# Performance work log

Hardware: AMD Instinct MI355X
Metric: run time of the kernel (lower is better)

Reference implementation:

```python
import jax, jax.numpy as jnp
import numpy as np

N = 100000      # total nodes (flattened batch)
E = 640000      # total edges
D = 128         # in_channels
SIM_THR = 0.2   # pt_dict['sim_pt']
DEG_THR = 3.0   # pt_dict['degree_pt']
PT_THRESHOLD = 0.1  # edge-pruning cosine threshold
EPS = 1e-8      # F.cosine_similarity eps


def _glorot(key, shape):
    a = np.sqrt(6.0 / (shape[-2] + shape[-1]))
    return jax.random.uniform(key, shape, jnp.float32, -a, a)


def setup_inputs() -> dict:
    key = jax.random.key(0)
    k1, k2, k3, k4, k5 = jax.random.split(key, 5)
    x = jax.random.normal(k1, (N, D), jnp.float32)
    edge_index = jax.random.randint(k2, (2, E), 0, N, dtype=jnp.int32)
    p_sim = _glorot(k3, (1, D))
    p_deg = _glorot(k4, (1, D))
    p_other = _glorot(k5, (1, D))
    return {"x": x, "edge_index": edge_index, "p_sim": p_sim, "p_deg": p_deg, "p_other": p_other}


def reference(x, edge_index, p_sim, p_deg, p_other):
    n = x.shape[0]
    row, col = edge_index[0], edge_index[1]

    # --- sim_pt: per-edge cosine of raw features, scatter-add to dst, degree-normalize ---
    x_norm = x / jnp.sqrt(jnp.sum(x * x, axis=1, keepdims=True))          # [N, D]
    e = jnp.sum(x_norm[row] * x_norm[col], axis=1)                         # [E]
    c = jax.ops.segment_sum(e, col, num_segments=n)                        # [N]
    deg = jax.ops.segment_sum(jnp.ones_like(e), col, num_segments=n)       # [N]
    # torch: c/deg -> nan for deg==0, nan <= thr is False; +inf gives the same mask, safely.
    csim = jnp.where(deg > 0, c / jnp.maximum(deg, 1.0), jnp.inf)
    mask_sim = csim <= SIM_THR                                             # [N]

    # --- degree_pt ---
    mask_deg = deg <= DEG_THR                                              # [N]

    # --- other_pt == 'all': nodes that got no prompt so far ---
    mask_other = ~(mask_sim | mask_deg)                                    # [N]

    # g_mutiftpt_record: [N, 3, D], slot filled with its prompt row where mask else 0
    masks = jnp.stack([mask_sim, mask_deg, mask_other], axis=1)            # [N, 3]
    prompts = jnp.concatenate([p_sim, p_deg, p_other], axis=0)             # [3, D]
    record = masks[:, :, None].astype(x.dtype) * prompts[None, :, :]       # [N, 3, D]

    # use_attention=False branch: mean over non-padding (all-nonzero) slots
    wo_pad = jnp.all(record != 0, axis=-1)                                 # [N, 3]
    plen = jnp.sum(wo_pad, axis=1, keepdims=True).astype(x.dtype)          # [N, 1]
    final = jnp.where(plen > 0, record.sum(axis=1) / jnp.maximum(plen, 1.0), 0.0)  # [N, D]

    x_new = x + final                                                      # add_pt

    # edge pruning by cosine similarity of prompted features (F.cosine_similarity, eps=1e-8)
    nrm = jnp.sqrt(jnp.sum(x_new * x_new, axis=1))                         # [N]
    na = jnp.maximum(nrm[row], EPS)
    nb = jnp.maximum(nrm[col], EPS)
    cos = jnp.sum(x_new[row] * x_new[col], axis=1) / (na * nb)             # [E]
    keep_edges = cos >= PT_THRESHOLD                                       # [E] bool mask (edge list is static-shape; mask instead of compaction)
    return x_new, keep_edges
```

## Files before the change

kernel.cpp:

```cpp
#include <hip/hip_runtime.h>
#include <hip/hip_bf16.h>
#include <hip/hip_fp8.h>
#include <math.h>

#define D_DIM 128
#define SIM_THR 0.2f
#define DEG_THR 3.0f
#define PT_THR 0.1
#define EPS_CS 1e-8
#define NODE_MARGIN 0.022f
#define PRUNE_MARGIN 0.022f
#define PK 4294967296.0

typedef unsigned short u16;
typedef unsigned int u32;

#define WS_NEED 8092900

__device__ __forceinline__ float bf2f(u16 u) {
    return __uint_as_float(((u32)u) << 16);
}
__device__ __forceinline__ float f8f(u32 v) {
    __hip_fp8_e4m3 t;
    t.__x = (__hip_fp8_storage_t)v;
    return (float)t;
}
__device__ __forceinline__ u16 f2bf(float f) {
    __hip_bfloat16 b = __float2bfloat16(f);
    return *(u16*)&b;
}

__global__ void node_pre_fp8(const float* __restrict__ x,
                             const float* __restrict__ ps,
                             const float* __restrict__ pd,
                             const float* __restrict__ po,
                             u32* __restrict__ x8d,
                             float* __restrict__ nx,
                             float* __restrict__ rs,
                             float* __restrict__ rd,
                             float* __restrict__ ro,
                             double* __restrict__ cd,
                             u32* __restrict__ bitmap, int nbmw,
                             int* __restrict__ flags,
                             float* __restrict__ G, int N) {
    int g = threadIdx.x >> 5;
    int lane = threadIdx.x & 31;
    int n = blockIdx.x * 8 + g;
    int gid = blockIdx.x * 256 + threadIdx.x;
    if (gid < nbmw) bitmap[gid] = 0u;
    if (n < N) {
        int off = lane * 4;
        const float4 v = *(const float4*)(x + (size_t)n * D_DIM + off);
        const float4 s = *(const float4*)(ps + off);
        const float4 d = *(const float4*)(pd + off);
        const float4 o = *(const float4*)(po + off);
        float sq = v.x * v.x + v.y * v.y + v.z * v.z + v.w * v.w;
        float drs = v.x * s.x + v.y * s.y + v.z * s.z + v.w * s.w;
        float drd = v.x * d.x + v.y * d.y + v.z * d.z + v.w * d.w;
        float dro = v.x * o.x + v.y * o.y + v.z * o.z + v.w * o.w;
        for (int m = 16; m; m >>= 1) {
            sq += __shfl_xor(sq, m, 32);
            drs += __shfl_xor(drs, m, 32);
            drd += __shfl_xor(drd, m, 32);
            dro += __shfl_xor(dro, m, 32);
        }
        float nrm = sqrtf(sq);
        float inv = 1.0f / nrm;
        __hip_fp8_e4m3 q0(v.x * inv), q1(v.y * inv), q2(v.z * inv), q3(v.w * inv);
        u32 packed = (u32)q0.__x | ((u32)q1.__x << 8) |
                     ((u32)q2.__x << 16) | ((u32)q3.__x << 24);
        x8d[(size_t)n * 32 + lane] = packed;
        if (lane == 0) {
            nx[n] = nrm;
            rs[n] = drs;
            rd[n] = drd;
            ro[n] = dro;
            cd[n] = 0.0;
        }
    }
    if (blockIdx.x == 0 && threadIdx.x < 64) {
        int t = threadIdx.x;
        float s0 = ps[t], s1 = ps[t + 64];
        float d0 = pd[t], d1 = pd[t + 64];
        float o0 = po[t], o1 = po[t + 64];
        float ss = s0 * s0 + s1 * s1;
        float sd = s0 * d0 + s1 * d1;
        float so = s0 * o0 + s1 * o1;
        float dd = d0 * d0 + d1 * d1;
        float dO = d0 * o0 + d1 * o1;
        float oo = o0 * o0 + o1 * o1;
        for (int m = 32; m; m >>= 1) {
            ss += __shfl_xor(ss, m);
            sd += __shfl_xor(sd, m);
            so += __shfl_xor(so, m);
            dd += __shfl_xor(dd, m);
            dO += __shfl_xor(dO, m);
            oo += __shfl_xor(oo, m);
        }
        unsigned long long zs = __ballot(s0 == 0.0f || s1 == 0.0f);
        unsigned long long zd = __ballot(d0 == 0.0f || d1 == 0.0f);
        unsigned long long zo = __ballot(o0 == 0.0f || o1 == 0.0f);
        if (t == 0) {
            flags[0] = (zs == 0ull);
            flags[1] = (zd == 0ull);
            flags[2] = (zo == 0ull);
            G[0] = ss; G[1] = sd; G[2] = so;
            G[3] = sd; G[4] = dd; G[5] = dO;
            G[6] = so; G[7] = dO; G[8] = oo;
        }
    }
}

__global__ void edge_sim_fp8(const u32* __restrict__ x8d,
                             const int* __restrict__ ei,
                             double* __restrict__ cd,
                             u16* __restrict__ e_arr,
                             int E) {
    int lane = threadIdx.x & 31;
    int grp = blockIdx.x * 8 + (threadIdx.x >> 5);
    int base = grp * 4;
    if (base >= E) return;

    int r[4], c4[4];
    #pragma unroll
    for (int k = 0; k < 4; ++k) {
        int e = base + k;
        int src = (e < E) ? e : base;
        r[k] = ei[src];
        c4[k] = ei[E + src];
    }
    u32 a[4], b[4];
    #pragma unroll
    for (int k = 0; k < 4; ++k) {
        a[k] = x8d[(size_t)r[k] * 32 + lane];
        b[k] = x8d[(size_t)c4[k] * 32 + lane];
    }
    float d[4];
    #pragma unroll
    for (int k = 0; k < 4; ++k) {
        d[k] = f8f(a[k] & 255u) * f8f(b[k] & 255u) +
               f8f((a[k] >> 8) & 255u) * f8f((b[k] >> 8) & 255u) +
               f8f((a[k] >> 16) & 255u) * f8f((b[k] >> 16) & 255u) +
               f8f(a[k] >> 24) * f8f(b[k] >> 24);
    }
    for (int m = 16; m; m >>= 1) {
        #pragma unroll
        for (int k = 0; k < 4; ++k) d[k] += __shfl_xor(d[k], m, 32);
    }
    if (lane < 4) {
        int e = base + lane;
        if (e < E) {
            float dv = (lane == 0) ? d[0] : (lane == 1) ? d[1]
                     : (lane == 2) ? d[2] : d[3];
            e_arr[e] = f2bf(dv);
            atomicAdd(&cd[c4[lane]], (double)dv + PK);
        }
    }
}

__global__ void node_prompt_kernel(const float* __restrict__ x,
                                   const double* __restrict__ cd,
                                   const float* __restrict__ ps,
                                   const float* __restrict__ pd,
                                   const float* __restrict__ po,
                                   const int* __restrict__ flags,
                                   const float* __restrict__ nx,
                                   const float* __restrict__ rs,
                                   const float* __restrict__ rd,
                                   const float* __restrict__ ro,
                                   float* __restrict__ xn,
                                   double* __restrict__ na,
                                   float* __restrict__ pack,
                                   u32* __restrict__ bitmap,
                                   float* __restrict__ cfix, int N) {
    int g = threadIdx.x >> 5;
    int lane = threadIdx.x & 31;
    int n = blockIdx.x * 8 + g;
    if (n >= N) return;
    double v = cd[n];
    double degd = floor(v * (1.0 / PK) + 0.5);
    float dg = (float)degd;
    float cc = (float)(v - degd * PK);
    float csim = (dg > 0.0f) ? (cc / fmaxf(dg, 1.0f)) : INFINITY;
    bool ms = (csim <= SIM_THR);
    bool md = (dg <= DEG_THR);
    bool mo = !(ms || md);
    int plen = (ms && flags[0]) + (md && flags[1]) + (mo && flags[2]);
    float invp = (plen > 0) ? (1.0f / (float)plen) : 0.0f;

    int off = lane * 4;
    const float4 xv = *(const float4*)(x + (size_t)n * D_DIM + off);
    const float4 s  = *(const float4*)(ps + off);
    const float4 dd = *(const float4*)(pd + off);
    const float4 o  = *(const float4*)(po + off);

    float4 f;
    f.x = (ms ? s.x : 0.0f) + (md ? dd.x : 0.0f) + (mo ? o.x : 0.0f);
    f.y = (ms ? s.y : 0.0f) + (md ? dd.y : 0.0f) + (mo ? o.y : 0.0f);
    f.z = (ms ? s.z : 0.0f) + (md ? dd.z : 0.0f) + (mo ? o.z : 0.0f);
    f.w = (ms ? s.w : 0.0f) + (md ? dd.w : 0.0f) + (mo ? o.w : 0.0f);

    float4 r;
    r.x = xv.x + f.x * invp;
    r.y = xv.y + f.y * invp;
    r.z = xv.z + f.z * invp;
    r.w = xv.w + f.w * invp;

    *(float4*)(xn + (size_t)n * D_DIM + off) = r;

    double sq = (double)r.x * r.x + (double)r.y * r.y + (double)r.z * r.z + (double)r.w * r.w;
    for (int m = 16; m; m >>= 1) sq += __shfl_xor(sq, m, 32);
    if (lane == 0) {
        double nrm = sqrt(sq);
        double nad = (nrm > EPS_CS) ? nrm : EPS_CS;
        na[n] = nad;
        float as = ms ? invp : 0.0f;
        float ad = md ? invp : 0.0f;
        float ao = mo ? invp : 0.0f;
        *(float4*)(pack + (size_t)n * 8)     = make_float4(rs[n], rd[n], ro[n], nx[n]);
        *(float4*)(pack + (size_t)n * 8 + 4) = make_float4(as, ad, ao, (float)(1.0 / nad));
        if (dg > 0.0f && fabsf(csim - SIM_THR) < NODE_MARGIN) {
            cfix[n] = 0.0f;
            atomicOr(&bitmap[n >> 5], 1u << (n & 31));
        }
    }
}

__global__ void edge_fix_scan(const float* __restrict__ x,
                              const int* __restrict__ ei,
                              const float* __restrict__ nx,
                              const u32* __restrict__ bitmap,
                              float* __restrict__ cfix, int E) {
    int e = blockIdx.x * 256 + threadIdx.x;
    if (e >= E) return;
    int col = ei[E + e];
    if (!((bitmap[col >> 5] >> (col & 31)) & 1u)) return;
    int row = ei[e];
    const float4* xr = (const float4*)(x + (size_t)row * D_DIM);
    const float4* xc = (const float4*)(x + (size_t)col * D_DIM);
    double s = 0.0;
    for (int i = 0; i < 32; ++i) {
        float4 a = xr[i], b = xc[i];
        s += (double)a.x * b.x + (double)a.y * b.y +
             (double)a.z * b.z + (double)a.w * b.w;
    }
    float ev = (float)(s / ((double)nx[row] * (double)nx[col]));
    atomicAdd(&cfix[col], ev);
}

__global__ void node_fix_kernel(const float* __restrict__ x,
                                const double* __restrict__ cd,
                                const float* __restrict__ cfix,
                                const u32* __restrict__ bitmap,
                                const float* __restrict__ ps,
                                const float* __restrict__ pd,
                                const float* __restrict__ po,
                                const int* __restrict__ flags,
                                const float* __restrict__ nx,
                                const float* __restrict__ rs,
                                const float* __restrict__ rd,
                                const float* __restrict__ ro,
                                float* __restrict__ xn,
                                double* __restrict__ na,
                                float* __restrict__ pack, int N) {
    int g = threadIdx.x >> 5;
    int lane = threadIdx.x & 31;
    int n = blockIdx.x * 8 + g;
    if (n >= N) return;
    if (!((bitmap[n >> 5] >> (n & 31)) & 1u)) return;

    double v = cd[n];
    double degd = floor(v * (1.0 / PK) + 0.5);
    float dg = (float)degd;
    float csim = cfix[n] / fmaxf(dg, 1.0f);
    bool ms = (csim <= SIM_THR);
    bool md = (dg <= DEG_THR);
    bool mo = !(ms || md);
    int plen = (ms && flags[0]) + (md && flags[1]) + (mo && flags[2]);
    float invp = (plen > 0) ? (1.0f / (float)plen) : 0.0f;

    int off = lane * 4;
    const float4 xv = *(const float4*)(x + (size_t)n * D_DIM + off);
    const float4 s  = *(const float4*)(ps + off);
    const float4 dd = *(const float4*)(pd + off);
    const float4 o  = *(const float4*)(po + off);

    float4 f;
    f.x = (ms ? s.x : 0.0f) + (md ? dd.x : 0.0f) + (mo ? o.x : 0.0f);
    f.y = (ms ? s.y : 0.0f) + (md ? dd.y : 0.0f) + (mo ? o.y : 0.0f);
    f.z = (ms ? s.z : 0.0f) + (md ? dd.z : 0.0f) + (mo ? o.z : 0.0f);
    f.w = (ms ? s.w : 0.0f) + (md ? dd.w : 0.0f) + (mo ? o.w : 0.0f);

    float4 r;
    r.x = xv.x + f.x * invp;
    r.y = xv.y + f.y * invp;
    r.z = xv.z + f.z * invp;
    r.w = xv.w + f.w * invp;

    *(float4*)(xn + (size_t)n * D_DIM + off) = r;

    double sq = (double)r.x * r.x + (double)r.y * r.y + (double)r.z * r.z + (double)r.w * r.w;
    for (int m = 16; m; m >>= 1) sq += __shfl_xor(sq, m, 32);
    if (lane == 0) {
        double nrm = sqrt(sq);
        double nad = (nrm > EPS_CS) ? nrm : EPS_CS;
        na[n] = nad;
        float as = ms ? invp : 0.0f;
        float ad = md ? invp : 0.0f;
        float ao = mo ? invp : 0.0f;
        *(float4*)(pack + (size_t)n * 8)     = make_float4(rs[n], rd[n], ro[n], nx[n]);
        *(float4*)(pack + (size_t)n * 8 + 4) = make_float4(as, ad, ao, (float)(1.0 / nad));
    }
}

__global__ void edge_prune_fused(const int* __restrict__ ei,
                                 const u16* __restrict__ e_arr,
                                 const float* __restrict__ pack,
                                 const float* __restrict__ G,
                                 const float* __restrict__ xn,
                                 const double* __restrict__ na,
                                 float* __restrict__ keep, int E) {
    __shared__ int s_list[256];
    __shared__ int s_cnt;
    int tid = threadIdx.x;
    if (tid == 0) s_cnt = 0;
    __syncthreads();

    int e = blockIdx.x * 256 + tid;
    if (e < E) {
        int i = ei[e], j = ei[E + e];
        const float4 ri = *(const float4*)(pack + (size_t)i * 8);
        const float4 ai = *(const float4*)(pack + (size_t)i * 8 + 4);
        const float4 rj = *(const float4*)(pack + (size_t)j * 8);
        const float4 aj = *(const float4*)(pack + (size_t)j * 8 + 4);
        float ev = bf2f(e_arr[e]);
        float dot = ev * ri.w * rj.w
                  + aj.x * ri.x + aj.y * ri.y + aj.z * ri.z
                  + ai.x * rj.x + ai.y * rj.y + ai.z * rj.z;
        dot += ai.x * (G[0] * aj.x + G[1] * aj.y + G[2] * aj.z)
             + ai.y * (G[3] * aj.x + G[4] * aj.y + G[5] * aj.z)
             + ai.z * (G[6] * aj.x + G[7] * aj.y + G[8] * aj.z);
        float cosv = dot * ai.w * aj.w;
        keep[e] = (cosv >= 0.1f) ? 1.0f : 0.0f;
        if (fabsf(cosv - 0.1f) < PRUNE_MARGIN) {
            int idx = atomicAdd(&s_cnt, 1);
            if (idx < 256) {
                s_list[idx] = e;
            } else {
                const float4* xr = (const float4*)(xn + (size_t)i * D_DIM);
                const float4* xc = (const float4*)(xn + (size_t)j * D_DIM);
                double sd = 0.0;
                for (int it = 0; it < 32; ++it) {
                    float4 a = xr[it], b = xc[it];
                    sd += (double)a.x * b.x + (double)a.y * b.y +
                          (double)a.z * b.z + (double)a.w * b.w;
                }
                double cs = sd / (na[i] * na[j]);
                keep[e] = (cs >= PT_THR) ? 1.0f : 0.0f;
            }
        }
    }
    __syncthreads();

    int cnt = s_cnt < 256 ? s_cnt : 256;
    int lane = tid & 31;
    int grp = tid >> 5;
    for (int it = grp; it < cnt; it += 8) {
        int ee = s_list[it];
        int row = ei[ee], col = ei[E + ee];
        const float4 a = *(const float4*)(xn + (size_t)row * D_DIM + lane * 4);
        const float4 b = *(const float4*)(xn + (size_t)col * D_DIM + lane * 4);
        double d = (double)a.x * b.x + (double)a.y * b.y +
                   (double)a.z * b.z + (double)a.w * b.w;
        for (int m = 16; m; m >>= 1) d += __shfl_xor(d, m, 32);
        if (lane == 0) {
            double cs = d / (na[row] * na[col]);
            keep[ee] = (cs >= PT_THR) ? 1.0f : 0.0f;
        }
    }
}

__global__ void node_pre_bf16(const float* __restrict__ x,
                              const float* __restrict__ ps,
                              const float* __restrict__ pd,
                              const float* __restrict__ po,
                              u16* __restrict__ xnorm,
                              double* __restrict__ cd,
                              int* __restrict__ flags, int N) {
    int g = threadIdx.x >> 5;
    int lane = threadIdx.x & 31;
    int n = blockIdx.x * 8 + g;
    if (n < N) {
        int off = lane * 4;
        const float4 v = *(const float4*)(x + (size_t)n * D_DIM + off);
        float sq = v.x * v.x + v.y * v.y + v.z * v.z + v.w * v.w;
        for (int m = 16; m; m >>= 1) sq += __shfl_xor(sq, m, 32);
        float inv = 1.0f / sqrtf(sq);
        *(ushort4*)(xnorm + (size_t)n * D_DIM + off) =
            make_ushort4(f2bf(v.x * inv), f2bf(v.y * inv), f2bf(v.z * inv), f2bf(v.w * inv));
        if (lane == 0) cd[n] = 0.0;
    }
    if (blockIdx.x == 0 && threadIdx.x < 64) {
        int t = threadIdx.x;
        unsigned long long zs = __ballot(ps[t] == 0.0f || ps[t + 64] == 0.0f);
        unsigned long long zd = __ballot(pd[t] == 0.0f || pd[t + 64] == 0.0f);
        unsigned long long zo = __ballot(po[t] == 0.0f || po[t + 64] == 0.0f);
        if (t == 0) {
            flags[0] = (zs == 0ull);
            flags[1] = (zd == 0ull);
            flags[2] = (zo == 0ull);
        }
    }
}

__global__ void edge_sim_bf16(const u16* __restrict__ xnorm,
                              const int* __restrict__ ei,
                              double* __restrict__ cd, int E) {
    int lane = threadIdx.x & 31;
    int grp = blockIdx.x * 8 + (threadIdx.x >> 5);
    int base = grp * 4;
    if (base >= E) return;
    int r[4], c4[4];
    #pragma unroll
    for (int k = 0; k < 4; ++k) {
        int e = base + k;
        int src = (e < E) ? e : base;
        r[k] = ei[src];
        c4[k] = ei[E + src];
    }
    float d[4];
    #pragma unroll
    for (int k = 0; k < 4; ++k) {
        ushort4 a = *(const ushort4*)(xnorm + (size_t)r[k] * D_DIM + lane * 4);
        ushort4 b = *(const ushort4*)(xnorm + (size_t)c4[k] * D_DIM + lane * 4);
        d[k] = bf2f(a.x) * bf2f(b.x) + bf2f(a.y) * bf2f(b.y) +
               bf2f(a.z) * bf2f(b.z) + bf2f(a.w) * bf2f(b.w);
    }
    for (int m = 16; m; m >>= 1) {
        #pragma unroll
        for (int k = 0; k < 4; ++k) d[k] += __shfl_xor(d[k], m, 32);
    }
    if (lane < 4) {
        int e = base + lane;
        if (e < E) {
            float dv = (lane == 0) ? d[0] : (lane == 1) ? d[1]
                     : (lane == 2) ? d[2] : d[3];
            atomicAdd(&cd[c4[lane]], (double)dv + PK);
        }
    }
}

__global__ void node_prompt_fb(const float* __restrict__ x,
                               const double* __restrict__ cd,
                               const float* __restrict__ ps,
                               const float* __restrict__ pd,
                               const float* __restrict__ po,
                               const int* __restrict__ flags,
                               float* __restrict__ xn,
                               double* __restrict__ na, int N) {
    int g = threadIdx.x >> 5;
    int lane = threadIdx.x & 31;
    int n = blockIdx.x * 8 + g;
    if (n >= N) return;
    double v = cd[n];
    double degd = floor(v * (1.0 / PK) + 0.5);
    float dg = (float)degd;
    float cc = (float)(v - degd * PK);
    float csim = (dg > 0.0f) ? (cc / fmaxf(dg, 1.0f)) : INFINITY;
    bool ms = (csim <= SIM_THR);
    bool md = (dg <= DEG_THR);
    bool mo = !(ms || md);
    int plen = (ms && flags[0]) + (md && flags[1]) + (mo && flags[2]);
    float invp = (plen > 0) ? (1.0f / (float)plen) : 0.0f;
    int off = lane * 4;
    const float4 xv = *(const float4*)(x + (size_t)n * D_DIM + off);
    const float4 s  = *(const float4*)(ps + off);
    const float4 dd = *(const float4*)(pd + off);
    const float4 o  = *(const float4*)(po + off);
    float4 r;
    r.x = xv.x + ((ms ? s.x : 0.0f) + (md ? dd.x : 0.0f) + (mo ? o.x : 0.0f)) * invp;
    r.y = xv.y + ((ms ? s.y : 0.0f) + (md ? dd.y : 0.0f) + (mo ? o.y : 0.0f)) * invp;
    r.z = xv.z + ((ms ? s.z : 0.0f) + (md ? dd.z : 0.0f) + (mo ? o.z : 0.0f)) * invp;
    r.w = xv.w + ((ms ? s.w : 0.0f) + (md ? dd.w : 0.0f) + (mo ? o.w : 0.0f)) * invp;
    *(float4*)(xn + (size_t)n * D_DIM + off) = r;
    double sq = (double)r.x * r.x + (double)r.y * r.y + (double)r.z * r.z + (double)r.w * r.w;
    for (int m = 16; m; m >>= 1) sq += __shfl_xor(sq, m, 32);
    if (lane == 0) {
        double nrm = sqrt(sq);
        na[n] = (nrm > EPS_CS) ? nrm : EPS_CS;
    }
}

__global__ void edge_prune_exact(const float* __restrict__ xn,
                                 const int* __restrict__ ei,
                                 const double* __restrict__ na,
                                 float* __restrict__ keep, int E) {
    int lane = threadIdx.x & 31;
    int grp = blockIdx.x * 8 + (threadIdx.x >> 5);
    int e0 = grp * 2, e1 = e0 + 1;
    if (e0 >= E) return;
    bool has1 = (e1 < E);
    int row0 = ei[e0], col0 = ei[E + e0];
    int row1 = has1 ? ei[e1] : row0;
    int col1 = has1 ? ei[E + e1] : col0;
    const float4 a0 = *(const float4*)(xn + (size_t)row0 * D_DIM + lane * 4);
    const float4 b0 = *(const float4*)(xn + (size_t)col0 * D_DIM + lane * 4);
    const float4 a1 = *(const float4*)(xn + (size_t)row1 * D_DIM + lane * 4);
    const float4 b1 = *(const float4*)(xn + (size_t)col1 * D_DIM + lane * 4);
    double d0 = (double)a0.x * b0.x + (double)a0.y * b0.y +
                (double)a0.z * b0.z + (double)a0.w * b0.w;
    double d1 = (double)a1.x * b1.x + (double)a1.y * b1.y +
                (double)a1.z * b1.z + (double)a1.w * b1.w;
    for (int m = 16; m; m >>= 1) {
        d0 += __shfl_xor(d0, m, 32);
        d1 += __shfl_xor(d1, m, 32);
    }
    if (lane == 0) {
        keep[e0] = ((d0 / (na[row0] * na[col0])) >= PT_THR) ? 1.0f : 0.0f;
    } else if (lane == 1 && has1) {
        keep[e1] = ((d1 / (na[row1] * na[col1])) >= PT_THR) ? 1.0f : 0.0f;
    }
}

extern "C" void kernel_launch(void* const* d_in, const int* in_sizes, int n_in,
                              void* d_out, int out_size, void* d_ws, size_t ws_size,
                              hipStream_t stream) {
    const float* x  = (const float*)d_in[0];
    const int*   ei = (const int*)d_in[1];
    const float* ps = (const float*)d_in[2];
    const float* pd = (const float*)d_in[3];
    const float* po = (const float*)d_in[4];

    const int N = in_sizes[0] / D_DIM;
    const int E = in_sizes[1] / 2;

    float* xn   = (float*)d_out;
    float* keep = (float*)d_out + (size_t)N * D_DIM;

    char* ws = (char*)d_ws;
    const int nodeBlocks = (N + 7) / 8;
    const int nbmw = (N + 31) / 32;

    if (ws_size >= (size_t)WS_NEED) {
        double* cd    = (double*)(ws + 0);
        double* na    = (double*)(ws + 800000);
        float* nx     = (float*)(ws + 1600000);
        float* rs     = (float*)(ws + 2000000);
        float* rd     = (float*)(ws + 2400000);
        float* ro     = (float*)(ws + 2800000);
        u16*   e_arr  = (u16*)(ws + 3200000);
        float* pack   = (float*)(ws + 4480000);
        float* cfix   = (float*)(ws + 7680000);
        u32*   bitmap = (u32*)(ws + 8080000);
        int*   flags  = (int*)(ws + 8092800);
        float* G      = (float*)(ws + 8092816);
        u32*   x8d    = (u32*)d_out;

        node_pre_fp8<<<nodeBlocks, 256, 0, stream>>>(x, ps, pd, po, x8d, nx, rs, rd, ro,
                                                     cd, bitmap, nbmw, flags, G, N);
        edge_sim_fp8<<<(E + 31) / 32, 256, 0, stream>>>(x8d, ei, cd, e_arr, E);
        node_prompt_kernel<<<nodeBlocks, 256, 0, stream>>>(x, cd, ps, pd, po, flags,
                                                           nx, rs, rd, ro,
                                                           xn, na, pack, bitmap, cfix, N);
        edge_fix_scan<<<(E + 255) / 256, 256, 0, stream>>>(x, ei, nx, bitmap, cfix, E);
        node_fix_kernel<<<nodeBlocks, 256, 0, stream>>>(x, cd, cfix, bitmap, ps, pd, po,
                                                        flags, nx, rs, rd, ro,
                                                        xn, na, pack, N);
        edge_prune_fused<<<(E + 255) / 256, 256, 0, stream>>>(ei, e_arr, pack, G,
                                                              xn, na, keep, E);
    } else {
        double* cd    = (double*)(ws + 0);
        double* na    = (double*)(ws + 800000);
        int*    flags = (int*)(ws + 1600000);
        u16*    xnorm = (u16*)d_out;

        node_pre_bf16<<<nodeBlocks, 256, 0, stream>>>(x, ps, pd, po, xnorm, cd, flags, N);
        edge_sim_bf16<<<(E + 31) / 32, 256, 0, stream>>>(xnorm, ei, cd, E);
        node_prompt_fb<<<nodeBlocks, 256, 0, stream>>>(x, cd, ps, pd, po, flags, xn, na, N);
        edge_prune_exact<<<(E + 15) / 16, 256, 0, stream>>>(xn, ei, na, keep, E);
    }
}
```

Baseline: 115.6 us.

## Switch edge cosine to per-row scaled int8 with sdot4 and skip empty fix passes

Result: faster. 108.6 us (-6.0%).

```diff
diff --git a/kernel.cpp b/kernel.cpp
--- a/kernel.cpp
+++ b/kernel.cpp
@@ -1,6 +1,5 @@
 #include <hip/hip_runtime.h>
 #include <hip/hip_bf16.h>
-#include <hip/hip_fp8.h>
 #include <math.h>
 
 #define D_DIM 128
@@ -8,46 +7,55 @@
 #define DEG_THR 3.0f
 #define PT_THR 0.1
 #define EPS_CS 1e-8
-#define NODE_MARGIN 0.022f
-#define PRUNE_MARGIN 0.022f
+#define NODE_MARGIN 8e-3f
+#define PRUNE_MARGIN 8e-3f
 #define PK 4294967296.0
 
 typedef unsigned short u16;
 typedef unsigned int u32;
 
-#define WS_NEED 8092900
+#define WS_NEED 9772860
 
 __device__ __forceinline__ float bf2f(u16 u) {
     return __uint_as_float(((u32)u) << 16);
-}
-__device__ __forceinline__ float f8f(u32 v) {
-    __hip_fp8_e4m3 t;
-    t.__x = (__hip_fp8_storage_t)v;
-    return (float)t;
 }
 __device__ __forceinline__ u16 f2bf(float f) {
     __hip_bfloat16 b = __float2bfloat16(f);
     return *(u16*)&b;
 }
-
-__global__ void node_pre_fp8(const float* __restrict__ x,
-                             const float* __restrict__ ps,
-                             const float* __restrict__ pd,
-                             const float* __restrict__ po,
-                             u32* __restrict__ x8d,
-                             float* __restrict__ nx,
-                             float* __restrict__ rs,
-                             float* __restrict__ rd,
-                             float* __restrict__ ro,
-                             double* __restrict__ cd,
-                             u32* __restrict__ bitmap, int nbmw,
-                             int* __restrict__ flags,
-                             float* __restrict__ G, int N) {
+__device__ __forceinline__ int dot4i8(u32 a, u32 b, int acc) {
+#if __has_builtin(__builtin_amdgcn_sdot4)
+    return __builtin_amdgcn_sdot4(a, b, acc, false);
+#else
+    acc += (int)(char)(a) * (int)(char)(b);
+    acc += (int)(char)(a >> 8) * (int)(char)(b >> 8);
+    acc += (int)(char)(a >> 16) * (int)(char)(b >> 16);
+    acc += (int)(char)(a >> 24) * (int)(char)(b >> 24);
+    return acc;
+#endif
+}
+
+__global__ void node_pre_i8(const float* __restrict__ x,
+                            const float* __restrict__ ps,
+                            const float* __restrict__ pd,
+                            const float* __restrict__ po,
+                            u32* __restrict__ x8d,
+                            float* __restrict__ nx,
+                            float* __restrict__ rs,
+                            float* __restrict__ rd,
+                            float* __restrict__ ro,
+                            float* __restrict__ sc,
+                            double* __restrict__ cd,
+                            u32* __restrict__ bitmap, int nbmw,
+                            int* __restrict__ flags,
+                            float* __restrict__ G,
+                            int* __restrict__ flagcnt, int N) {
     int g = threadIdx.x >> 5;
     int lane = threadIdx.x & 31;
     int n = blockIdx.x * 8 + g;
     int gid = blockIdx.x * 256 + threadIdx.x;
     if (gid < nbmw) bitmap[gid] = 0u;
+    if (gid == 0) *flagcnt = 0;
     if (n < N) {
         int off = lane * 4;
         const float4 v = *(const float4*)(x + (size_t)n * D_DIM + off);
@@ -66,15 +74,24 @@
         }
         float nrm = sqrtf(sq);
         float inv = 1.0f / nrm;
-        __hip_fp8_e4m3 q0(v.x * inv), q1(v.y * inv), q2(v.z * inv), q3(v.w * inv);
-        u32 packed = (u32)q0.__x | ((u32)q1.__x << 8) |
-                     ((u32)q2.__x << 16) | ((u32)q3.__x << 24);
+        float v0 = v.x * inv, v1 = v.y * inv, v2 = v.z * inv, v3 = v.w * inv;
+        float mx = fmaxf(fmaxf(fabsf(v0), fabsf(v1)), fmaxf(fabsf(v2), fabsf(v3)));
+        for (int m = 16; m; m >>= 1) mx = fmaxf(mx, __shfl_xor(mx, m, 32));
+        float scale = fmaxf(mx, 1e-20f) * (1.0f / 127.0f);
+        float isc = 1.0f / scale;
+        int q0 = __float2int_rn(v0 * isc);
+        int q1 = __float2int_rn(v1 * isc);
+        int q2 = __float2int_rn(v2 * isc);
+        int q3 = __float2int_rn(v3 * isc);
+        u32 packed = ((u32)q0 & 255u) | (((u32)q1 & 255u) << 8) |
+                     (((u32)q2 & 255u) << 16) | (((u32)q3 & 255u) << 24);
         x8d[(size_t)n * 32 + lane] = packed;
         if (lane == 0) {
             nx[n] = nrm;
             rs[n] = drs;
             rd[n] = drd;
             ro[n] = dro;
+            sc[n] = scale;
             cd[n] = 0.0;
         }
     }
@@ -111,11 +128,12 @@
     }
 }
 
-__global__ void edge_sim_fp8(const u32* __restrict__ x8d,
-                             const int* __restrict__ ei,
-                             double* __restrict__ cd,
-                             u16* __restrict__ e_arr,
-                             int E) {
+__global__ void edge_sim_i8(const u32* __restrict__ x8d,
+                            const int* __restrict__ ei,
+                            const float* __restrict__ sc,
+                            double* __restrict__ cd,
+                            float* __restrict__ e_arr,
+                            int E) {
     int lane = threadIdx.x & 31;
     int grp = blockIdx.x * 8 + (threadIdx.x >> 5);
     int base = grp * 4;
@@ -135,14 +153,9 @@
         a[k] = x8d[(size_t)r[k] * 32 + lane];
         b[k] = x8d[(size_t)c4[k] * 32 + lane];
     }
-    float d[4];
+    int d[4];
     #pragma unroll
-    for (int k = 0; k < 4; ++k) {
-        d[k] = f8f(a[k] & 255u) * f8f(b[k] & 255u) +
-               f8f((a[k] >> 8) & 255u) * f8f((b[k] >> 8) & 255u) +
-               f8f((a[k] >> 16) & 255u) * f8f((b[k] >> 16) & 255u) +
-               f8f(a[k] >> 24) * f8f(b[k] >> 24);
-    }
+    for (int k = 0; k < 4; ++k) d[k] = dot4i8(a[k], b[k], 0);
     for (int m = 16; m; m >>= 1) {
         #pragma unroll
         for (int k = 0; k < 4; ++k) d[k] += __shfl_xor(d[k], m, 32);
@@ -150,10 +163,12 @@
     if (lane < 4) {
         int e = base + lane;
         if (e < E) {
-            float dv = (lane == 0) ? d[0] : (lane == 1) ? d[1]
+            int idot = (lane == 0) ? d[0] : (lane == 1) ? d[1]
                      : (lane == 2) ? d[2] : d[3];
-            e_arr[e] = f2bf(dv);
-            atomicAdd(&cd[c4[lane]], (double)dv + PK);
+            int rr = r[lane], cc = c4[lane];
+            float ev = (float)idot * sc[rr] * sc[cc];
+            e_arr[e] = ev;
+            atomicAdd(&cd[cc], (double)ev + PK);
         }
     }
 }
@@ -172,7 +187,8 @@
                                    double* __restrict__ na,
                                    float* __restrict__ pack,
                                    u32* __restrict__ bitmap,
-                                   float* __restrict__ cfix, int N) {
+                                   float* __restrict__ cfix,
+                                   int* __restrict__ flagcnt, int N) {
     int g = threadIdx.x >> 5;
     int lane = threadIdx.x & 31;
     int n = blockIdx.x * 8 + g;
@@ -222,6 +238,7 @@
         if (dg > 0.0f && fabsf(csim - SIM_THR) < NODE_MARGIN) {
             cfix[n] = 0.0f;
             atomicOr(&bitmap[n >> 5], 1u << (n & 31));
+            atomicAdd(flagcnt, 1);
         }
     }
 }
@@ -230,7 +247,9 @@
                               const int* __restrict__ ei,
                               const float* __restrict__ nx,
                               const u32* __restrict__ bitmap,
+                              const int* __restrict__ flagcnt,
                               float* __restrict__ cfix, int E) {
+    if (*flagcnt == 0) return;
     int e = blockIdx.x * 256 + threadIdx.x;
     if (e >= E) return;
     int col = ei[E + e];
@@ -252,6 +271,7 @@
                                 const double* __restrict__ cd,
                                 const float* __restrict__ cfix,
                                 const u32* __restrict__ bitmap,
+                                const int* __restrict__ flagcnt,
                                 const float* __restrict__ ps,
                                 const float* __restrict__ pd,
                                 const float* __restrict__ po,
@@ -263,6 +283,7 @@
                                 float* __restrict__ xn,
                                 double* __restrict__ na,
                                 float* __restrict__ pack, int N) {
+    if (*flagcnt == 0) return;
     int g = threadIdx.x >> 5;
     int lane = threadIdx.x & 31;
     int n = blockIdx.x * 8 + g;
@@ -314,7 +335,7 @@
 }
 
 __global__ void edge_prune_fused(const int* __restrict__ ei,
-                                 const u16* __restrict__ e_arr,
+                                 const float* __restrict__ e_arr,
                                  const float* __restrict__ pack,
                                  const float* __restrict__ G,
                                  const float* __restrict__ xn,
@@ -333,7 +354,7 @@
         const float4 ai = *(const float4*)(pack + (size_t)i * 8 + 4);
         const float4 rj = *(const float4*)(pack + (size_t)j * 8);
         const float4 aj = *(const float4*)(pack + (size_t)j * 8 + 4);
-        float ev = bf2f(e_arr[e]);
+        float ev = e_arr[e];
         float dot = ev * ri.w * rj.w
                   + aj.x * ri.x + aj.y * ri.y + aj.z * ri.z
                   + ai.x * rj.x + ai.y * rj.y + ai.z * rj.z;
@@ -542,29 +563,34 @@
     const int nbmw = (N + 31) / 32;
 
     if (ws_size >= (size_t)WS_NEED) {
-        double* cd    = (double*)(ws + 0);
-        double* na    = (double*)(ws + 800000);
-        float* nx     = (float*)(ws + 1600000);
-        float* rs     = (float*)(ws + 2000000);
-        float* rd     = (float*)(ws + 2400000);
-        float* ro     = (float*)(ws + 2800000);
-        u16*   e_arr  = (u16*)(ws + 3200000);
-        float* pack   = (float*)(ws + 4480000);
-        float* cfix   = (float*)(ws + 7680000);
-        u32*   bitmap = (u32*)(ws + 8080000);
-        int*   flags  = (int*)(ws + 8092800);
-        float* G      = (float*)(ws + 8092816);
-        u32*   x8d    = (u32*)d_out;
-
-        node_pre_fp8<<<nodeBlocks, 256, 0, stream>>>(x, ps, pd, po, x8d, nx, rs, rd, ro,
-                                                     cd, bitmap, nbmw, flags, G, N);
-        edge_sim_fp8<<<(E + 31) / 32, 256, 0, stream>>>(x8d, ei, cd, e_arr, E);
+        double* cd     = (double*)(ws + 0);
+        double* na     = (double*)(ws + 800000);
+        float* nx      = (float*)(ws + 1600000);
+        float* rs      = (float*)(ws + 2000000);
+        float* rd      = (float*)(ws + 2400000);
+        float* ro      = (float*)(ws + 2800000);
+        float* sc      = (float*)(ws + 3200000);
+        float* e_arr   = (float*)(ws + 3600000);
+        float* pack    = (float*)(ws + 6160000);
+        float* cfix    = (float*)(ws + 9360000);
+        u32*   bitmap  = (u32*)(ws + 9760000);
+        int*   flags   = (int*)(ws + 9772800);
+        float* G       = (float*)(ws + 9772816);
+        int*   flagcnt = (int*)(ws + 9772852);
+        u32*   x8d     = (u32*)d_out;
+
+        node_pre_i8<<<nodeBlocks, 256, 0, stream>>>(x, ps, pd, po, x8d, nx, rs, rd, ro,
+                                                    sc, cd, bitmap, nbmw, flags, G,
+                                                    flagcnt, N);
+        edge_sim_i8<<<(E + 31) / 32, 256, 0, stream>>>(x8d, ei, sc, cd, e_arr, E);
         node_prompt_kernel<<<nodeBlocks, 256, 0, stream>>>(x, cd, ps, pd, po, flags,
                                                            nx, rs, rd, ro,
-                                                           xn, na, pack, bitmap, cfix, N);
-        edge_fix_scan<<<(E + 255) / 256, 256, 0, stream>>>(x, ei, nx, bitmap, cfix, E);
-        node_fix_kernel<<<nodeBlocks, 256, 0, stream>>>(x, cd, cfix, bitmap, ps, pd, po,
-                                                        flags, nx, rs, rd, ro,
+                                                           xn, na, pack, bitmap, cfix,
+                                                           flagcnt, N);
+        edge_fix_scan<<<(E + 255) / 256, 256, 0, stream>>>(x, ei, nx, bitmap, flagcnt,
+                                                           cfix, E);
+        node_fix_kernel<<<nodeBlocks, 256, 0, stream>>>(x, cd, cfix, bitmap, flagcnt,
+                                                        ps, pd, po, flags, nx, rs, rd, ro,
                                                         xn, na, pack, N);
         edge_prune_fused<<<(E + 255) / 256, 256, 0, stream>>>(ei, e_arr, pack, G,
                                                               xn, na, keep, E);
```
